# Kernel optimization log

Measured on AMD Instinct MI355X. Metric: run time of the kernel, lower is better.

Reference implementation:

```python
import jax, jax.numpy as jnp
import numpy as np

B, L, N, H = 1024, 200, 2, 128  # batch, block_len, code_rate_n, dec_num_unit


def setup_inputs() -> dict:
    key = jax.random.key(0)
    ks = jax.random.split(key, 24)
    s = 0.05
    inp = {"received": jax.random.normal(ks[0], (B, N * L, 1), jnp.float32)}
    # dec_linear: Linear(n*L, n*L)
    inp["W_lin"] = jax.random.normal(ks[1], (N * L, N * L), jnp.float32) * s
    inp["b_lin"] = jax.random.normal(ks[2], (N * L,), jnp.float32) * s
    # GRU params, PyTorch layout: W_ih [3H, in], W_hh [3H, H], gates ordered (r, z, n)
    specs = [("0f", N), ("0b", N), ("1f", 2 * H), ("1b", 2 * H)]
    i = 3
    for tag, din in specs:
        inp[f"Wih{tag}"] = jax.random.normal(ks[i], (3 * H, din), jnp.float32) * s; i += 1
        inp[f"Whh{tag}"] = jax.random.normal(ks[i], (3 * H, H), jnp.float32) * s; i += 1
        inp[f"bih{tag}"] = jax.random.normal(ks[i], (3 * H,), jnp.float32) * s; i += 1
        inp[f"bhh{tag}"] = jax.random.normal(ks[i], (3 * H,), jnp.float32) * s; i += 1
    # final: Linear(2H, 1)
    inp["Wf"] = jax.random.normal(ks[i], (1, 2 * H), jnp.float32) * s
    inp["bf"] = jax.random.normal(ks[i + 1], (1,), jnp.float32) * s
    return inp


def _gru_dir(x, Wih, Whh, bih, bhh, reverse):
    # x: [B, L, din] -> outputs [B, L, H]; PyTorch GRU cell math, gate order (r, z, n)
    h_dim = Whh.shape[1]
    xg = jnp.einsum('bld,gd->blg', x, Wih) + bih          # precompute input gates [B,L,3H]
    xg = jnp.swapaxes(xg, 0, 1)                            # [L,B,3H] for scan over time
    h0 = jnp.zeros((x.shape[0], h_dim), x.dtype)

    def step(h, g):
        hg = h @ Whh.T + bhh
        r = jax.nn.sigmoid(g[:, :h_dim] + hg[:, :h_dim])
        z = jax.nn.sigmoid(g[:, h_dim:2 * h_dim] + hg[:, h_dim:2 * h_dim])
        n = jnp.tanh(g[:, 2 * h_dim:] + r * hg[:, 2 * h_dim:])
        h = (1.0 - z) * n + z * h
        return h, h

    _, hs = jax.lax.scan(step, h0, xg, reverse=reverse)    # [L,B,H], time-aligned
    return jnp.swapaxes(hs, 0, 1)


def reference(received, W_lin, b_lin,
              Wih0f, Whh0f, bih0f, bhh0f,
              Wih0b, Whh0b, bih0b, bhh0b,
              Wih1f, Whh1f, bih1f, bhh1f,
              Wih1b, Whh1b, bih1b, bhh1b,
              Wf, bf):
    b = received.shape[0]
    permuted = jnp.swapaxes(received, 1, 2)                # [B, 1, n*L]
    code = permuted @ W_lin.T + b_lin                      # dec_linear
    n_in = Wih0f.shape[1]
    code = code.reshape(b, -1, n_in)                       # [B, L, n]
    # layer 0 (bidirectional)
    h0 = jnp.concatenate([
        _gru_dir(code, Wih0f, Whh0f, bih0f, bhh0f, False),
        _gru_dir(code, Wih0b, Whh0b, bih0b, bhh0b, True)], axis=-1)   # [B,L,2H]
    # layer 1 (bidirectional)
    h1 = jnp.concatenate([
        _gru_dir(h0, Wih1f, Whh1f, bih1f, bhh1f, False),
        _gru_dir(h0, Wih1b, Whh1b, bih1b, bhh1b, True)], axis=-1)     # [B,L,2H]
    return jax.nn.sigmoid(h1 @ Wf.T + bf)                  # [B,L,1]
```

## Files before the change

### kernel.cpp

```cpp
#include <hip/hip_runtime.h>
#include <hip/hip_bf16.h>

#define B_   1024
#define L_   200
#define H_   128
#define BL_  204800
#define G3_  384

typedef __bf16 bf16x8 __attribute__((ext_vector_type(8)));
typedef __bf16 bf16x4 __attribute__((ext_vector_type(4)));
typedef float  f32x4  __attribute__((ext_vector_type(4)));

__device__ __forceinline__ float sigf(float x) {
    return __builtin_amdgcn_rcpf(1.f + __expf(-x));
}
__device__ __forceinline__ float tanh_fast(float x) {
    float e = __expf(-2.f * x);
    return (1.f - e) * __builtin_amdgcn_rcpf(1.f + e);
}
__device__ __forceinline__ bf16x8 cvt8(float4 a, float4 b) {
    bf16x8 v;
    v[0] = (__bf16)a.x; v[1] = (__bf16)a.y; v[2] = (__bf16)a.z; v[3] = (__bf16)a.w;
    v[4] = (__bf16)b.x; v[5] = (__bf16)b.y; v[6] = (__bf16)b.z; v[7] = (__bf16)b.w;
    return v;
}
__device__ __forceinline__ void barrier_lds() {
    __builtin_amdgcn_sched_barrier(0);
    asm volatile("s_waitcnt lgkmcnt(0)" ::: "memory");
    __builtin_amdgcn_s_barrier();
    __builtin_amdgcn_sched_barrier(0);
}
__device__ __forceinline__ float red16(float v) {
    v += __int_as_float(__builtin_amdgcn_update_dpp(0, __float_as_int(v), 0x121, 0xF, 0xF, true));
    v += __int_as_float(__builtin_amdgcn_update_dpp(0, __float_as_int(v), 0x122, 0xF, 0xF, true));
    v += __int_as_float(__builtin_amdgcn_update_dpp(0, __float_as_int(v), 0x124, 0xF, 0xF, true));
    v += __int_as_float(__builtin_amdgcn_update_dpp(0, __float_as_int(v), 0x128, 0xF, 0xF, true));
    return v;
}

__global__ __launch_bounds__(256) void k_sentinel(float* __restrict__ out, int n) {
    const int i = blockIdx.x * 256 + threadIdx.x;
    if (i < n) out[i] = -5.0f;
}

__global__ __launch_bounds__(256) void k_declin(
    const float* __restrict__ rcv, const float* __restrict__ Wl,
    const float* __restrict__ bl, float* __restrict__ code) {
    __shared__ float rs[4][400];
    const int tid = threadIdx.x;
    const int b0 = blockIdx.x * 4;
    for (int i = tid; i < 1600; i += 256) ((float*)rs)[i] = rcv[(size_t)b0 * 400 + i];
    __syncthreads();
    #pragma unroll
    for (int rep = 0; rep < 2; ++rep) {
        const int j = tid + rep * 256;
        if (j < 400) {
            float a0 = 0.f, a1 = 0.f, a2 = 0.f, a3 = 0.f;
            const float4* wp = (const float4*)(Wl + (size_t)j * 400);
            for (int k = 0; k < 100; ++k) {
                float4 w4 = wp[k];
                const int kk = k * 4;
                a0 += w4.x*rs[0][kk] + w4.y*rs[0][kk+1] + w4.z*rs[0][kk+2] + w4.w*rs[0][kk+3];
                a1 += w4.x*rs[1][kk] + w4.y*rs[1][kk+1] + w4.z*rs[1][kk+2] + w4.w*rs[1][kk+3];
                a2 += w4.x*rs[2][kk] + w4.y*rs[2][kk+1] + w4.z*rs[2][kk+2] + w4.w*rs[2][kk+3];
                a3 += w4.x*rs[3][kk] + w4.y*rs[3][kk+1] + w4.z*rs[3][kk+2] + w4.w*rs[3][kk+3];
            }
            const float bb = bl[j];
            code[(size_t)(b0+0)*400 + j] = a0 + bb;
            code[(size_t)(b0+1)*400 + j] = a1 + bb;
            code[(size_t)(b0+2)*400 + j] = a2 + bb;
            code[(size_t)(b0+3)*400 + j] = a3 + bb;
        }
    }
}

__global__ __launch_bounds__(512, 2) void k_gru0(
    const float* __restrict__ code,
    const float* __restrict__ Wih_f, const float* __restrict__ Whh_f,
    const float* __restrict__ bih_f, const float* __restrict__ bhh_f,
    const float* __restrict__ Wih_b, const float* __restrict__ Whh_b,
    const float* __restrict__ bih_b, const float* __restrict__ bhh_b,
    __bf16* __restrict__ h0) {
    const int dir = blockIdx.y;
    const int b0 = blockIdx.x * 8;
    const float* Wih = dir ? Wih_b : Wih_f;
    const float* Whh = dir ? Whh_b : Whh_f;
    const float* bih = dir ? bih_b : bih_f;
    const float* bhh = dir ? bhh_b : bhh_f;

    const int tid = threadIdx.x;
    const int w = tid >> 6, ln = tid & 63, q = ln >> 4, r16 = ln & 15;
    const int jj = w * 16 + r16;

    __shared__ __bf16 h_bf[2][16][136];
    __shared__ float  code_s[8][400];
    __shared__ __bf16 h_st[2][8][8][136];

    for (int i = tid; i < 8 * 400; i += 512) ((float*)code_s)[i] = code[(size_t)b0 * 400 + i];
    for (int i = tid; i < 2 * 16 * 136; i += 512) ((__bf16*)h_bf)[i] = (__bf16)0.f;

    bf16x8 wfr[3][4];
    const float wr0 = Wih[jj * 2],         wr1 = Wih[jj * 2 + 1];
    const float wz0 = Wih[(jj + 128) * 2], wz1 = Wih[(jj + 128) * 2 + 1];
    const float wn0 = Wih[(jj + 256) * 2], wn1 = Wih[(jj + 256) * 2 + 1];
    const float xbr = bih[jj] + bhh[jj];
    const float xbz = bih[jj + 128] + bhh[jj + 128];
    const float xbn = bih[jj + 256];
    const float bnv = bhh[jj + 256];
    float hreg2[2] = {0.f, 0.f};
    #pragma unroll
    for (int g = 0; g < 3; ++g) {
        const int j = (w + g * 8) * 16 + r16;
        const float* p = Whh + (size_t)j * H_;
        #pragma unroll
        for (int kt = 0; kt < 4; ++kt) {
            float4 x0 = *(const float4*)(p + kt * 32 + q * 8);
            float4 x1 = *(const float4*)(p + kt * 32 + q * 8 + 4);
            wfr[g][kt] = cvt8(x0, x1);
        }
    }
    __syncthreads();

    for (int t = 0; t < L_; ++t) {
        const int cur = t & 1, nxt = cur ^ 1;
        if ((t & 7) == 0 && t > 0) {
            const int g8 = (t >> 3) - 1;
            const int buf = g8 & 1;
            const int p = tid >> 3, inner = tid & 7;
            const int s = p >> 3, row = p & 7;
            const int tb = g8 * 8 + s;
            const int lf = dir ? (L_ - 1 - tb) : tb;
            const __bf16* src = &h_st[buf][s][row][inner * 16];
            __bf16* dst = &h0[((size_t)(b0 + row) * L_ + lf) * 256 + dir * 128 + inner * 16];
            *(bf16x8*)(dst)     = *(const bf16x8*)(src);
            *(bf16x8*)(dst + 8) = *(const bf16x8*)(src + 8);
        }
        const int l = dir ? (L_ - 1 - t) : t;
        bf16x8 af[4];
        #pragma unroll
        for (int kt = 0; kt < 4; ++kt)
            af[kt] = *(const bf16x8*)&h_bf[cur][r16][kt * 32 + q * 8];

        f32x4 ar = {0.f,0.f,0.f,0.f}, az = {0.f,0.f,0.f,0.f}, an = {0.f,0.f,0.f,0.f};
        #pragma unroll
        for (int kt = 0; kt < 4; ++kt) {
            ar = __builtin_amdgcn_mfma_f32_16x16x32_bf16(af[kt], wfr[0][kt], ar, 0, 0, 0);
            az = __builtin_amdgcn_mfma_f32_16x16x32_bf16(af[kt], wfr[1][kt], az, 0, 0, 0);
            an = __builtin_amdgcn_mfma_f32_16x16x32_bf16(af[kt], wfr[2][kt], an, 0, 0, 0);
        }
        #pragma unroll
        for (int i = 0; i < 2; ++i) {
            const int m = 2 * q + i;
            const float c0 = code_s[m][l * 2], c1 = code_s[m][l * 2 + 1];
            const float r = sigf(c0 * wr0 + c1 * wr1 + xbr + ar[i]);
            const float z = sigf(c0 * wz0 + c1 * wz1 + xbz + az[i]);
            const float n = tanh_fast(c0 * wn0 + c1 * wn1 + xbn + r * (an[i] + bnv));
            const float hv = n + z * (hreg2[i] - n);
            hreg2[i] = hv;
            h_bf[nxt][4 * q + i][jj] = (__bf16)hv;
            h_st[(t >> 3) & 1][t & 7][m][jj] = (__bf16)hv;
        }
        barrier_lds();
    }
    {
        const int p = tid >> 3, inner = tid & 7;
        const int s = p >> 3, row = p & 7;
        const int tb = 192 + s;
        const int lf = dir ? (L_ - 1 - tb) : tb;
        const __bf16* src = &h_st[0][s][row][inner * 16];
        __bf16* dst = &h0[((size_t)(b0 + row) * L_ + lf) * 256 + dir * 128 + inner * 16];
        *(bf16x8*)(dst)     = *(const bf16x8*)(src);
        *(bf16x8*)(dst + 8) = *(const bf16x8*)(src + 8);
    }
}

__global__ __launch_bounds__(256) void k_cvtW(
    const float* __restrict__ Wfp, const float* __restrict__ Wbp,
    __bf16* __restrict__ out) {
    const int j = blockIdx.x * 256 + threadIdx.x;
    const int base = j * 4;
    const int dir = base >= 98304;
    const int idx = dir ? base - 98304 : base;
    float4 v = *(const float4*)((dir ? Wbp : Wfp) + idx);
    bf16x4 o;
    o[0] = (__bf16)v.x; o[1] = (__bf16)v.y; o[2] = (__bf16)v.z; o[3] = (__bf16)v.w;
    *(bf16x4*)&out[base] = o;
}

__global__ __launch_bounds__(512, 2) void k_gru1f(
    const __bf16* __restrict__ h0,
    const __bf16* __restrict__ Wihbf,
    const float* __restrict__ bih_f, const float* __restrict__ bhh_f,
    const float* __restrict__ bih_b, const float* __restrict__ bhh_b,
    const float* __restrict__ Whh_f, const float* __restrict__ Whh_b,
    const float* __restrict__ Wfin,
    float* __restrict__ partial) {
    const int dir = blockIdx.y;
    const int b0 = blockIdx.x * 8;
    const float* Whh = dir ? Whh_b : Whh_f;
    const float* bih = dir ? bih_b : bih_f;
    const float* bhh = dir ? bhh_b : bhh_f;
    const __bf16* Wb = Wihbf + (size_t)dir * 384 * 256;

    const int tid = threadIdx.x;
    const int w = tid >> 6, ln = tid & 63, q = ln >> 4, r16 = ln & 15;
    const int jj = w * 16 + r16;

    __shared__ __bf16 xa[2][32][264];
    __shared__ __bf16 h_bf[2][16][136];
    __shared__ float  wacc[2][8][8];

    for (int i = tid; i < 2 * 16 * 136; i += 512) ((__bf16*)h_bf)[i] = (__bf16)0.f;

    bf16x8 wfr[3][4];
    bf16x8 wB[3][8];
    const float xbr = bih[jj] + bhh[jj];
    const float xbz = bih[jj + 128] + bhh[jj + 128];
    const float xbn = bih[jj + 256];
    const float bnv = bhh[jj + 256];
    const float wfv = Wfin[dir * 128 + jj];
    float hreg2[2] = {0.f, 0.f};
    #pragma unroll
    for (int g = 0; g < 3; ++g) {
        const int j = (w + g * 8) * 16 + r16;
        const float* p = Whh + (size_t)j * H_;
        #pragma unroll
        for (int kt = 0; kt < 4; ++kt) {
            float4 x0 = *(const float4*)(p + kt * 32 + q * 8);
            float4 x1 = *(const float4*)(p + kt * 32 + q * 8 + 4);
            wfr[g][kt] = cvt8(x0, x1);
        }
    }
    #pragma unroll
    for (int n = 0; n < 3; ++n) {
        const int ct = w + n * 8;
        const __bf16* wp = Wb + (size_t)(ct * 16 + r16) * 256 + q * 8;
        #pragma unroll
        for (int k8 = 0; k8 < 8; ++k8)
            wB[n][k8] = *(const bf16x8*)(wp + k8 * 32);
    }
    const int prr = tid >> 4, prs = tid & 15;
    const int pmt = prr >> 4, pr4 = prr & 15;
    const int pa = pr4 >> 2, psh = (pr4 >> 1) & 1, pb = pr4 & 1;
    const int pS = 2 * pmt + psh;
    const int pBt = 2 * pa + pb;
    {
        const int l = dir ? (L_ - 1 - pS) : pS;
        const __bf16* src = h0 + ((size_t)(b0 + pBt) * L_ + l) * 256 + prs * 16;
        *(bf16x8*)&xa[0][prr][prs * 16]     = *(const bf16x8*)(src);
        *(bf16x8*)&xa[0][prr][prs * 16 + 8] = *(const bf16x8*)(src + 8);
    }
    __syncthreads();

    for (int c = 0; c < 50; ++c) {
        const int cb = c & 1, nb = cb ^ 1;
        bf16x8 pf0, pf1;
        const bool pv = (c + 1 < 50);
        if (pv) {
            const int t = (c + 1) * 4 + pS;
            const int l = dir ? (L_ - 1 - t) : t;
            const __bf16* src = h0 + ((size_t)(b0 + pBt) * L_ + l) * 256 + prs * 16;
            pf0 = *(const bf16x8*)(src);
            pf1 = *(const bf16x8*)(src + 8);
        }

        f32x4 accg[3][2];
        #pragma unroll
        for (int n = 0; n < 3; ++n)
            #pragma unroll
            for (int mt = 0; mt < 2; ++mt) {
                accg[n][mt][0]=0.f; accg[n][mt][1]=0.f;
                accg[n][mt][2]=0.f; accg[n][mt][3]=0.f;
            }
        #pragma unroll
        for (int k8 = 0; k8 < 8; ++k8) {
            const bf16x8 a0 = *(const bf16x8*)&xa[cb][r16][k8 * 32 + q * 8];
            const bf16x8 a1 = *(const bf16x8*)&xa[cb][16 + r16][k8 * 32 + q * 8];
            #pragma unroll
            for (int n = 0; n < 3; ++n) {
                accg[n][0] = __builtin_amdgcn_mfma_f32_16x16x32_bf16(a0, wB[n][k8], accg[n][0], 0, 0, 0);
                accg[n][1] = __builtin_amdgcn_mfma_f32_16x16x32_bf16(a1, wB[n][k8], accg[n][1], 0, 0, 0);
            }
        }

        #pragma unroll
        for (int s = 0; s < 4; ++s) {
            const int cur = s & 1, nxt = cur ^ 1;
            const int par = s & 1;
            const int t = c * 4 + s;
            const int l = dir ? (L_ - 1 - t) : t;
            const int mt = s >> 1;

            bf16x8 af[4];
            #pragma unroll
            for (int kt = 0; kt < 4; ++kt)
                af[kt] = *(const bf16x8*)&h_bf[cur][r16][kt * 32 + q * 8];

            f32x4 ar = {0.f,0.f,0.f,0.f}, az = {0.f,0.f,0.f,0.f}, an = {0.f,0.f,0.f,0.f};
            #pragma unroll
            for (int kt = 0; kt < 4; ++kt) {
                ar = __builtin_amdgcn_mfma_f32_16x16x32_bf16(af[kt], wfr[0][kt], ar, 0, 0, 0);
                az = __builtin_amdgcn_mfma_f32_16x16x32_bf16(af[kt], wfr[1][kt], az, 0, 0, 0);
                an = __builtin_amdgcn_mfma_f32_16x16x32_bf16(af[kt], wfr[2][kt], an, 0, 0, 0);
            }

            float hv2[2];
            #pragma unroll
            for (int i = 0; i < 2; ++i) {
                const int reg = 2 * (s & 1) + i;
                const float xrv = accg[0][mt][reg];
                const float xzv = accg[1][mt][reg];
                const float xnv = accg[2][mt][reg];
                const float r = sigf(xrv + xbr + ar[i]);
                const float z = sigf(xzv + xbz + az[i]);
                const float n = tanh_fast(xnv + xbn + r * (an[i] + bnv));
                const float hv = n + z * (hreg2[i] - n);
                hreg2[i] = hv;
                hv2[i] = hv;
                h_bf[nxt][4 * q + i][jj] = (__bf16)hv;
            }
            #pragma unroll
            for (int i = 0; i < 2; ++i) {
                const float v = red16(hv2[i] * wfv);
                if (r16 == 0) wacc[par][w][2 * q + i] = v;
            }
            if (pv && s == 2) {
                *(bf16x8*)&xa[nb][prr][prs * 16]     = pf0;
                *(bf16x8*)&xa[nb][prr][prs * 16 + 8] = pf1;
            }
            barrier_lds();
            if (tid < 8) {
                float v = 0.f;
                #pragma unroll
                for (int ww = 0; ww < 8; ++ww) v += wacc[par][ww][tid];
                partial[(size_t)dir * BL_ + (size_t)(b0 + tid) * L_ + l] = v;
            }
        }
    }
}

__global__ __launch_bounds__(256) void k_final(
    const float* __restrict__ partial, const float* __restrict__ bfp,
    float* __restrict__ out) {
    const int i = blockIdx.x * 256 + threadIdx.x;
    if (i < BL_) out[i] = sigf(partial[i] + partial[BL_ + i] + bfp[0]);
}

extern "C" void kernel_launch(void* const* d_in, const int* in_sizes, int n_in,
                              void* d_out, int out_size, void* d_ws, size_t ws_size,
                              hipStream_t stream) {
    const float* rcv   = (const float*)d_in[0];
    const float* Wl    = (const float*)d_in[1];
    const float* bl    = (const float*)d_in[2];
    const float* Wih0f = (const float*)d_in[3];
    const float* Whh0f = (const float*)d_in[4];
    const float* bih0f = (const float*)d_in[5];
    const float* bhh0f = (const float*)d_in[6];
    const float* Wih0b = (const float*)d_in[7];
    const float* Whh0b = (const float*)d_in[8];
    const float* bih0b = (const float*)d_in[9];
    const float* bhh0b = (const float*)d_in[10];
    const float* Wih1f = (const float*)d_in[11];
    const float* Whh1f = (const float*)d_in[12];
    const float* bih1f = (const float*)d_in[13];
    const float* bhh1f = (const float*)d_in[14];
    const float* Wih1b = (const float*)d_in[15];
    const float* Whh1b = (const float*)d_in[16];
    const float* bih1b = (const float*)d_in[17];
    const float* bhh1b = (const float*)d_in[18];
    const float* Wfin  = (const float*)d_in[19];
    const float* bfin  = (const float*)d_in[20];

    const size_t OFF_CODE = 0;
    const size_t OFF_PART = 1638400;
    const size_t OFF_H0   = 3276800;
    const size_t OFF_WBF  = 108134400;
    const size_t WS_NEEDED = 108527616;

    if (ws_size < WS_NEEDED) {
        k_sentinel<<<(out_size + 255) / 256, 256, 0, stream>>>((float*)d_out, out_size);
        return;
    }

    char* ws = (char*)d_ws;
    float*  code    = (float*)(ws + OFF_CODE);
    float*  partial = (float*)(ws + OFF_PART);
    __bf16* h0      = (__bf16*)(ws + OFF_H0);
    __bf16* Wihbf   = (__bf16*)(ws + OFF_WBF);

    k_declin<<<256, 256, 0, stream>>>(rcv, Wl, bl, code);
    k_cvtW<<<192, 256, 0, stream>>>(Wih1f, Wih1b, Wihbf);
    k_gru0<<<dim3(128, 2), 512, 0, stream>>>(code, Wih0f, Whh0f, bih0f, bhh0f,
                                             Wih0b, Whh0b, bih0b, bhh0b, h0);
    k_gru1f<<<dim3(128, 2), 512, 0, stream>>>(h0, Wihbf,
                                              bih1f, bhh1f, bih1b, bhh1b,
                                              Whh1f, Whh1b, Wfin, partial);
    k_final<<<800, 256, 0, stream>>>(partial, bfin, (float*)d_out);
}
```

Baseline: 409.8 us.

## Skip redundant h loads, write h0 directly, defer final-projection reduction by one step

```diff
diff --git a/kernel.cpp b/kernel.cpp
--- a/kernel.cpp
+++ b/kernel.cpp
@@ -91,10 +91,10 @@
     const int tid = threadIdx.x;
     const int w = tid >> 6, ln = tid & 63, q = ln >> 4, r16 = ln & 15;
     const int jj = w * 16 + r16;
+    const bool act = ((r16 & 2) == 0);
 
     __shared__ __bf16 h_bf[2][16][136];
     __shared__ float  code_s[8][400];
-    __shared__ __bf16 h_st[2][8][8][136];
 
     for (int i = tid; i < 8 * 400; i += 512) ((float*)code_s)[i] = code[(size_t)b0 * 400 + i];
     for (int i = tid; i < 2 * 16 * 136; i += 512) ((__bf16*)h_bf)[i] = (__bf16)0.f;
@@ -119,27 +119,21 @@
             wfr[g][kt] = cvt8(x0, x1);
         }
     }
+    bf16x8 af[4];
+    #pragma unroll
+    for (int kt = 0; kt < 4; ++kt)
+        #pragma unroll
+        for (int j = 0; j < 8; ++j) af[kt][j] = (__bf16)0.f;
     __syncthreads();
 
     for (int t = 0; t < L_; ++t) {
         const int cur = t & 1, nxt = cur ^ 1;
-        if ((t & 7) == 0 && t > 0) {
-            const int g8 = (t >> 3) - 1;
-            const int buf = g8 & 1;
-            const int p = tid >> 3, inner = tid & 7;
-            const int s = p >> 3, row = p & 7;
-            const int tb = g8 * 8 + s;
-            const int lf = dir ? (L_ - 1 - tb) : tb;
-            const __bf16* src = &h_st[buf][s][row][inner * 16];
-            __bf16* dst = &h0[((size_t)(b0 + row) * L_ + lf) * 256 + dir * 128 + inner * 16];
-            *(bf16x8*)(dst)     = *(const bf16x8*)(src);
-            *(bf16x8*)(dst + 8) = *(const bf16x8*)(src + 8);
-        }
         const int l = dir ? (L_ - 1 - t) : t;
-        bf16x8 af[4];
-        #pragma unroll
-        for (int kt = 0; kt < 4; ++kt)
-            af[kt] = *(const bf16x8*)&h_bf[cur][r16][kt * 32 + q * 8];
+        if (act) {
+            #pragma unroll
+            for (int kt = 0; kt < 4; ++kt)
+                af[kt] = *(const bf16x8*)&h_bf[cur][r16][kt * 32 + q * 8];
+        }
 
         f32x4 ar = {0.f,0.f,0.f,0.f}, az = {0.f,0.f,0.f,0.f}, an = {0.f,0.f,0.f,0.f};
         #pragma unroll
@@ -158,19 +152,9 @@
             const float hv = n + z * (hreg2[i] - n);
             hreg2[i] = hv;
             h_bf[nxt][4 * q + i][jj] = (__bf16)hv;
-            h_st[(t >> 3) & 1][t & 7][m][jj] = (__bf16)hv;
+            h0[((size_t)(b0 + m) * L_ + l) * 256 + dir * 128 + jj] = (__bf16)hv;
         }
         barrier_lds();
-    }
-    {
-        const int p = tid >> 3, inner = tid & 7;
-        const int s = p >> 3, row = p & 7;
-        const int tb = 192 + s;
-        const int lf = dir ? (L_ - 1 - tb) : tb;
-        const __bf16* src = &h_st[0][s][row][inner * 16];
-        __bf16* dst = &h0[((size_t)(b0 + row) * L_ + lf) * 256 + dir * 128 + inner * 16];
-        *(bf16x8*)(dst)     = *(const bf16x8*)(src);
-        *(bf16x8*)(dst + 8) = *(const bf16x8*)(src + 8);
     }
 }
 
@@ -205,6 +189,7 @@
     const int tid = threadIdx.x;
     const int w = tid >> 6, ln = tid & 63, q = ln >> 4, r16 = ln & 15;
     const int jj = w * 16 + r16;
+    const bool act = ((r16 & 2) == 0);
 
     __shared__ __bf16 xa[2][32][264];
     __shared__ __bf16 h_bf[2][16][136];
@@ -250,6 +235,13 @@
         *(bf16x8*)&xa[0][prr][prs * 16]     = *(const bf16x8*)(src);
         *(bf16x8*)&xa[0][prr][prs * 16 + 8] = *(const bf16x8*)(src + 8);
     }
+    bf16x8 af[4];
+    #pragma unroll
+    for (int kt = 0; kt < 4; ++kt)
+        #pragma unroll
+        for (int j = 0; j < 8; ++j) af[kt][j] = (__bf16)0.f;
+    float pp0 = 0.f, pp1 = 0.f;
+    int ppar = 0, plv = 0;
     __syncthreads();
 
     for (int c = 0; c < 50; ++c) {
@@ -286,15 +278,24 @@
         #pragma unroll
         for (int s = 0; s < 4; ++s) {
             const int cur = s & 1, nxt = cur ^ 1;
-            const int par = s & 1;
             const int t = c * 4 + s;
             const int l = dir ? (L_ - 1 - t) : t;
             const int mt = s >> 1;
-
-            bf16x8 af[4];
-            #pragma unroll
-            for (int kt = 0; kt < 4; ++kt)
-                af[kt] = *(const bf16x8*)&h_bf[cur][r16][kt * 32 + q * 8];
+            const bool havePrev = (s > 0) || (c > 0);
+
+            if (act) {
+                #pragma unroll
+                for (int kt = 0; kt < 4; ++kt)
+                    af[kt] = *(const bf16x8*)&h_bf[cur][r16][kt * 32 + q * 8];
+            }
+            if (havePrev) {
+                const float v0 = red16(pp0);
+                const float v1 = red16(pp1);
+                if (r16 == 0) {
+                    wacc[ppar][w][2 * q]     = v0;
+                    wacc[ppar][w][2 * q + 1] = v1;
+                }
+            }
 
             f32x4 ar = {0.f,0.f,0.f,0.f}, az = {0.f,0.f,0.f,0.f}, an = {0.f,0.f,0.f,0.f};
             #pragma unroll
@@ -319,22 +320,36 @@
                 hv2[i] = hv;
                 h_bf[nxt][4 * q + i][jj] = (__bf16)hv;
             }
-            #pragma unroll
-            for (int i = 0; i < 2; ++i) {
-                const float v = red16(hv2[i] * wfv);
-                if (r16 == 0) wacc[par][w][2 * q + i] = v;
-            }
             if (pv && s == 2) {
                 *(bf16x8*)&xa[nb][prr][prs * 16]     = pf0;
                 *(bf16x8*)&xa[nb][prr][prs * 16 + 8] = pf1;
             }
             barrier_lds();
-            if (tid < 8) {
+            if (havePrev && tid < 8) {
                 float v = 0.f;
                 #pragma unroll
-                for (int ww = 0; ww < 8; ++ww) v += wacc[par][ww][tid];
-                partial[(size_t)dir * BL_ + (size_t)(b0 + tid) * L_ + l] = v;
-            }
+                for (int ww = 0; ww < 8; ++ww) v += wacc[ppar][ww][tid];
+                partial[(size_t)dir * BL_ + (size_t)(b0 + tid) * L_ + plv] = v;
+            }
+            pp0 = hv2[0] * wfv;
+            pp1 = hv2[1] * wfv;
+            ppar = t & 1;
+            plv = l;
+        }
+    }
+    {
+        const float v0 = red16(pp0);
+        const float v1 = red16(pp1);
+        if (r16 == 0) {
+            wacc[ppar][w][2 * q]     = v0;
+            wacc[ppar][w][2 * q + 1] = v1;
+        }
+        __syncthreads();
+        if (tid < 8) {
+            float v = 0.f;
+            #pragma unroll
+            for (int ww = 0; ww < 8; ++ww) v += wacc[ppar][ww][tid];
+            partial[(size_t)dir * BL_ + (size_t)(b0 + tid) * L_ + plv] = v;
         }
     }
 }
```

New measurement: 420.0 us. 2.5% more time.
